# Performance work log

Hardware: AMD Instinct MI355X
Metric: run time of the kernel (lower is better)

Reference implementation:

```python
import jax, jax.numpy as jnp
import numpy as np

LR = 0.1  # inner-loop learning rate from `param - 0.1 * grad`

D = 4096          # memory width d; key/val are (1, d) per docstring
CTX = 512         # loss_context_size: number of keys per update step


def setup_inputs() -> dict:
    key = jax.random.key(0)
    k1, k2, k3 = jax.random.split(key, 3)
    W = jax.random.normal(k1, (D, D), dtype=jnp.float32) / np.sqrt(D)
    keys = jax.random.normal(k2, (CTX, D), dtype=jnp.float32)
    vals = jax.random.normal(k3, (CTX, D), dtype=jnp.float32)
    return {"W": W, "keys": keys, "vals": vals}


def reference(W, keys, vals):
    # OneStep.forward: preds_i = functional_forward(key_i, (W,)) = key_i @ W,
    # loss = MSE(preds, vals); new_W = W - 0.1 * dloss/dW.
    # The per-key loop is batched into a single (CTX, D) x (D, D) matmul.
    def loss_fn(Wp):
        preds = keys @ Wp  # (CTX, D)
        return jnp.mean((preds - vals) ** 2)

    g = jax.grad(loss_fn)(W)
    return W - LR * g
```

## Files before the change

kernel.cpp:

```cpp
#include <hip/hip_runtime.h>
#include <hip/hip_bf16.h>


typedef __bf16 bf16_t;
typedef __bf16 bf16x8 __attribute__((ext_vector_type(8)));
typedef float f32x4 __attribute__((ext_vector_type(4)));

#define D_DIM 4096
#define CTX_N 512
#define UPD_SCALE 9.5367431640625e-8f

__device__ __forceinline__ void gld16(const bf16_t* g, bf16_t* l) {
    __builtin_amdgcn_global_load_lds(
        (const __attribute__((address_space(1))) void*)g,
        (__attribute__((address_space(3))) void*)l, 16, 0, 0);
}

__device__ __forceinline__ void t_body2(
    float* tile, const float* __restrict__ src, bf16_t* __restrict__ dstT,
    bf16_t* __restrict__ dstN, int M, int N, int bx, int by)
{
    const int tid = threadIdx.x;
    const int C0 = bx * 64, R0 = by * 64;
    const int r  = tid >> 2, cs = (tid & 3) * 16;

    const float* s = src + (size_t)(R0 + r) * N + C0 + cs;
    float f[16];
#pragma unroll
    for (int u = 0; u < 4; ++u) {
        const float4 v = ((const float4*)s)[u];
        f[4 * u + 0] = v.x; f[4 * u + 1] = v.y; f[4 * u + 2] = v.z; f[4 * u + 3] = v.w;
    }
#pragma unroll
    for (int u = 0; u < 16; ++u) tile[r * 65 + cs + u] = f[u];

    if (dstN) {
        bf16x8 v0, v1;
#pragma unroll
        for (int u = 0; u < 8; ++u) { v0[u] = (bf16_t)f[u]; v1[u] = (bf16_t)f[8 + u]; }
        bf16_t* d = dstN + (size_t)(R0 + r) * N + C0 + cs;
        *(bf16x8*)d = v0; *(bf16x8*)(d + 8) = v1;
    }
    __syncthreads();

    bf16x8 o0, o1;
#pragma unroll
    for (int u = 0; u < 8; ++u) {
        o0[u] = (bf16_t)tile[(cs + u) * 65 + r];
        o1[u] = (bf16_t)tile[(cs + 8 + u) * 65 + r];
    }
    bf16_t* d = dstT + (size_t)(C0 + r) * M + R0 + cs;
    *(bf16x8*)d = o0; *(bf16x8*)(d + 8) = o1;
}

__global__ __launch_bounds__(256) void t_all(
    const float* __restrict__ W, const float* __restrict__ K,
    const float* __restrict__ V, bf16_t* __restrict__ Wt,
    bf16_t* __restrict__ Kt, bf16_t* __restrict__ Kb, bf16_t* __restrict__ Vt)
{
    __shared__ float tile[64 * 65];
    const int y = blockIdx.y;
    if (y < 64)      t_body2(tile, W, Wt, nullptr, D_DIM, D_DIM, blockIdx.x, y);
    else if (y < 72) t_body2(tile, K, Kt, Kb,      CTX_N, D_DIM, blockIdx.x, y - 64);
    else             t_body2(tile, V, Vt, nullptr, CTX_N, D_DIM, blockIdx.x, y - 72);
}



__global__ __launch_bounds__(512, 2) void k1_residual(
    const bf16_t* __restrict__ Wt, const bf16_t* __restrict__ Kb,
    const bf16_t* __restrict__ Vt, bf16_t* __restrict__ Rt)
{
    __shared__ __align__(16) bf16_t stg[2 * 12288];

    const int tid = threadIdx.x, wave = tid >> 6, lane = tid & 63;
    const int j0 = blockIdx.x * 128, c0 = blockIdx.y * 64;
    const int l15 = lane & 15, quad = lane >> 4;
    const int wm = wave >> 1, wn = wave & 1;

    f32x4 acc[2][2] = {};

    const int smi = wave >> 1, skk = wave & 1;
    const bf16_t* gA1 = Wt + (size_t)(j0 + smi * 16 + l15) * D_DIM + skk * 32 + quad * 8;
    const bf16_t* gA2 = gA1 + (size_t)64 * D_DIM;
    const bf16_t* gB  = Kb + (size_t)(c0 + smi * 16 + l15) * D_DIM + skk * 32 + quad * 8;

    auto stage = [&](int bsel, int t) {
        bf16_t* base = stg + bsel * 12288;
        gld16(gA1 + t * 64, base + (size_t)wave * 512 + lane * 8);
        gld16(gA2 + t * 64, base + (size_t)(8 + wave) * 512 + lane * 8);
        gld16(gB  + t * 64, base + 8192 + (size_t)wave * 512 + lane * 8);
    };

#define K1_COMPUTE(BSEL)                                                     \
    {                                                                        \
        const bf16_t* buf = stg + (BSEL) * 12288;                            \
        bf16x8 a[2][2], b[2][2];                                             \
        _Pragma("unroll")                                                    \
        for (int kk = 0; kk < 2; ++kk)                                       \
            _Pragma("unroll")                                                \
            for (int x = 0; x < 2; ++x) {                                    \
                a[x][kk] = *(const bf16x8*)(                                 \
                    buf + ((wm * 2 + x) * 2 + kk) * 512 + lane * 8);         \
                b[x][kk] = *(const bf16x8*)(                                 \
                    buf + 8192 + ((wn * 2 + x) * 2 + kk) * 512 + lane * 8);  \
            }                                                                \
        _Pragma("unroll")                                                    \
        for (int kk = 0; kk < 2; ++kk)                                       \
            _Pragma("unroll")                                                \
            for (int mi = 0; mi < 2; ++mi)                                   \
                _Pragma("unroll")                                            \
                for (int ni = 0; ni < 2; ++ni)                               \
                    acc[mi][ni] = __builtin_amdgcn_mfma_f32_16x16x32_bf16(   \
                        a[mi][kk], b[ni][kk], acc[mi][ni], 0, 0, 0);         \
    }

    stage(0, 0);
    __syncthreads();
#pragma unroll 1
    for (int t = 0; t < 62; t += 2) {
        stage(1, t + 1);
        __builtin_amdgcn_sched_barrier(0);
        K1_COMPUTE(0);
        __syncthreads();
        stage(0, t + 2);
        __builtin_amdgcn_sched_barrier(0);
        K1_COMPUTE(1);
        __syncthreads();
    }
    stage(1, 63);
    __builtin_amdgcn_sched_barrier(0);
    K1_COMPUTE(0);
    __syncthreads();
    K1_COMPUTE(1);

    {
        const size_t base =
            (size_t)(j0 + wm * 32 + quad * 4) * CTX_N + c0 + wn * 32 + l15;
#pragma unroll
        for (int mi = 0; mi < 2; ++mi)
#pragma unroll
            for (int r = 0; r < 4; ++r) {
                const size_t rowb = base + (size_t)(mi * 16 + r) * CTX_N;
#pragma unroll
                for (int ni = 0; ni < 2; ++ni) {
                    const size_t idx = rowb + ni * 16;
                    Rt[idx] = (bf16_t)(acc[mi][ni][r] - (float)Vt[idx]);
                }
            }
    }
}


#define K2_COMPUTE(BSEL)                                                     \
    {                                                                        \
        const bf16_t* As = (const bf16_t*)(smem + (BSEL) * 16384);           \
        const bf16_t* Bs = (const bf16_t*)(smem + (BSEL) * 16384 + 8192);    \
        bf16x8 af[4], bq[4];                                                 \
        _Pragma("unroll")                                                    \
        for (int mi = 0; mi < 4; ++mi)                                       \
            af[mi] = *(const bf16x8*)(As + (wi + mi * 16 + l15) * 32 + quad * 8); \
        _Pragma("unroll")                                                    \
        for (int ni = 0; ni < 4; ++ni)                                       \
            bq[ni] = *(const bf16x8*)(Bs + (wj + ni * 16 + l15) * 32 + quad * 8); \
        _Pragma("unroll")                                                    \
        for (int mi = 0; mi < 4; ++mi)                                       \
            _Pragma("unroll")                                                \
            for (int ni = 0; ni < 4; ++ni)                                   \
                acc[mi][ni] = __builtin_amdgcn_mfma_f32_16x16x32_bf16(       \
                    af[mi], bq[ni], acc[mi][ni], 0, 0, 0);                   \
    }

__global__ __launch_bounds__(256) void k2_update(
    const bf16_t* __restrict__ Kt, const bf16_t* __restrict__ Rt,
    const float* __restrict__ W, float* __restrict__ out)
{
    __shared__ __align__(16) char smem[32768];

    const int tid = threadIdx.x;

    const int id = blockIdx.x + 32 * blockIdx.y;
    const int xp = (id >> 3) & 31;
    const int yp = (id & 7) + 8 * (id >> 8);
    const int j0 = xp * 128, i0 = yp * 128;

    const int lane = tid & 63, wave = tid >> 6;
    const int wi = (wave >> 1) * 64, wj = (wave & 1) * 64;
    const int l15 = lane & 15, quad = lane >> 4;

    f32x4 acc[4][4] = {};

    const bf16_t* ga = Kt + (size_t)(i0 + (tid >> 2)) * CTX_N + (tid & 3) * 8;
    const bf16_t* gb = Rt + (size_t)(j0 + (tid >> 2)) * CTX_N + (tid & 3) * 8;

    auto stage = [&](int bsel, int cc) {
        bf16_t* la = (bf16_t*)(smem + bsel * 16384) + tid * 8;
        bf16_t* lb = (bf16_t*)(smem + bsel * 16384 + 8192) + tid * 8;
        gld16(ga + cc, la);
        gld16(ga + cc + (size_t)64 * CTX_N, la + 64 * 32);
        gld16(gb + cc, lb);
        gld16(gb + cc + (size_t)64 * CTX_N, lb + 64 * 32);
    };

    stage(0, 0);
    __syncthreads();
#pragma unroll 1
    for (int t = 1; t <= 13; t += 2) {
        stage(1, t * 32);
        __builtin_amdgcn_sched_barrier(0);
        K2_COMPUTE(0);
        __syncthreads();
        stage(0, (t + 1) * 32);
        __builtin_amdgcn_sched_barrier(0);
        K2_COMPUTE(1);
        __syncthreads();
    }
    stage(1, 15 * 32);
    __builtin_amdgcn_sched_barrier(0);
    K2_COMPUTE(0);
    __syncthreads();
    K2_COMPUTE(1);

    const size_t base = (size_t)(i0 + wi + quad * 4) * D_DIM + j0 + wj + l15;
    const float* wp = W + base;
    float*       op = out + base;

    float w0[16], w1[16];
#pragma unroll
    for (int r = 0; r < 4; ++r)
#pragma unroll
        for (int ni = 0; ni < 4; ++ni)
            w0[r * 4 + ni] = wp[(size_t)r * D_DIM + ni * 16];

#pragma unroll
    for (int mi = 0; mi < 4; ++mi) {
        float* wcur = (mi & 1) ? w1 : w0;
        float* wnxt = (mi & 1) ? w0 : w1;
        if (mi < 3) {
#pragma unroll
            for (int r = 0; r < 4; ++r)
#pragma unroll
                for (int ni = 0; ni < 4; ++ni)
                    wnxt[r * 4 + ni] =
                        wp[(size_t)((mi + 1) * 16 + r) * D_DIM + ni * 16];
        }
#pragma unroll
        for (int r = 0; r < 4; ++r)
#pragma unroll
            for (int ni = 0; ni < 4; ++ni)
                op[(size_t)(mi * 16 + r) * D_DIM + ni * 16] =
                    wcur[r * 4 + ni] - UPD_SCALE * acc[mi][ni][r];
    }
}

extern "C" void kernel_launch(void* const* d_in, const int* in_sizes, int n_in,
                              void* d_out, int out_size, void* d_ws, size_t ws_size,
                              hipStream_t stream) {
    const float* W = (const float*)d_in[0];
    const float* K = (const float*)d_in[1];
    const float* V = (const float*)d_in[2];
    float* out = (float*)d_out;

    char* ws = (char*)d_ws;
    bf16_t* Wt = (bf16_t*)(ws);
    bf16_t* Kt = (bf16_t*)(ws + (size_t)32 * 1024 * 1024);
    bf16_t* Kb = (bf16_t*)(ws + (size_t)36 * 1024 * 1024);
    bf16_t* Vt = (bf16_t*)(ws + (size_t)40 * 1024 * 1024);
    bf16_t* Rt = (bf16_t*)(ws + (size_t)44 * 1024 * 1024);

    t_all      <<<dim3(64, 80), 256, 0, stream>>>(W, K, V, Wt, Kt, Kb, Vt);
    k1_residual<<<dim3(32, 8),  512, 0, stream>>>(Wt, Kb, Vt, Rt);
    k2_update  <<<dim3(32, 32), 256, 0, stream>>>(Kt, Rt, W, out);
}
```

Measured before the change: 228.0 us.

## Shrink k1 block tile to 64x64 with XOR-swizzled LDS staging

```diff
diff --git a/kernel.cpp b/kernel.cpp
--- a/kernel.cpp
+++ b/kernel.cpp
@@ -67,44 +67,50 @@
 
 
 
-__global__ __launch_bounds__(512, 2) void k1_residual(
+__global__ __launch_bounds__(256, 2) void k1_residual(
     const bf16_t* __restrict__ Wt, const bf16_t* __restrict__ Kb,
     const bf16_t* __restrict__ Vt, bf16_t* __restrict__ Rt)
 {
-    __shared__ __align__(16) bf16_t stg[2 * 12288];
+    __shared__ __align__(16) bf16_t stg[16384];
 
     const int tid = threadIdx.x, wave = tid >> 6, lane = tid & 63;
-    const int j0 = blockIdx.x * 128, c0 = blockIdx.y * 64;
+    const int j0 = blockIdx.x * 64, c0 = blockIdx.y * 64;
     const int l15 = lane & 15, quad = lane >> 4;
     const int wm = wave >> 1, wn = wave & 1;
 
     f32x4 acc[2][2] = {};
 
-    const int smi = wave >> 1, skk = wave & 1;
-    const bf16_t* gA1 = Wt + (size_t)(j0 + smi * 16 + l15) * D_DIM + skk * 32 + quad * 8;
-    const bf16_t* gA2 = gA1 + (size_t)64 * D_DIM;
-    const bf16_t* gB  = Kb + (size_t)(c0 + smi * 16 + l15) * D_DIM + skk * 32 + quad * 8;
+    const int rl = lane >> 3;
+    const int sl = ((lane & 7) ^ rl) * 8;
+    const bf16_t* gA0 = Wt + (size_t)(j0 + wave * 8      + rl) * D_DIM + sl;
+    const bf16_t* gA1 = Wt + (size_t)(j0 + wave * 8 + 32 + rl) * D_DIM + sl;
+    const bf16_t* gB0 = Kb + (size_t)(c0 + wave * 8      + rl) * D_DIM + sl;
+    const bf16_t* gB1 = Kb + (size_t)(c0 + wave * 8 + 32 + rl) * D_DIM + sl;
 
     auto stage = [&](int bsel, int t) {
-        bf16_t* base = stg + bsel * 12288;
-        gld16(gA1 + t * 64, base + (size_t)wave * 512 + lane * 8);
-        gld16(gA2 + t * 64, base + (size_t)(8 + wave) * 512 + lane * 8);
-        gld16(gB  + t * 64, base + 8192 + (size_t)wave * 512 + lane * 8);
+        bf16_t* buf = stg + bsel * 8192;
+        gld16(gA0 + t * 64, buf + (size_t)wave * 512 + lane * 8);
+        gld16(gA1 + t * 64, buf + (size_t)(wave + 4) * 512 + lane * 8);
+        gld16(gB0 + t * 64, buf + 4096 + (size_t)wave * 512 + lane * 8);
+        gld16(gB1 + t * 64, buf + 4096 + (size_t)(wave + 4) * 512 + lane * 8);
     };
 
 #define K1_COMPUTE(BSEL)                                                     \
     {                                                                        \
-        const bf16_t* buf = stg + (BSEL) * 12288;                            \
+        const bf16_t* buf = stg + (BSEL) * 8192;                             \
+        const int r3 = l15 & 7, uh = l15 >> 3;                               \
         bf16x8 a[2][2], b[2][2];                                             \
         _Pragma("unroll")                                                    \
-        for (int kk = 0; kk < 2; ++kk)                                       \
+        for (int kk = 0; kk < 2; ++kk) {                                     \
+            const int slot = r3 * 8 + ((kk * 4 + quad) ^ r3);                \
             _Pragma("unroll")                                                \
             for (int x = 0; x < 2; ++x) {                                    \
-                a[x][kk] = *(const bf16x8*)(                                 \
-                    buf + ((wm * 2 + x) * 2 + kk) * 512 + lane * 8);         \
-                b[x][kk] = *(const bf16x8*)(                                 \
-                    buf + 8192 + ((wn * 2 + x) * 2 + kk) * 512 + lane * 8);  \
+                const int uA = wm * 4 + x * 2 + uh;                          \
+                const int uB = wn * 4 + x * 2 + uh;                          \
+                a[x][kk] = *(const bf16x8*)(buf + uA * 512 + slot * 8);      \
+                b[x][kk] = *(const bf16x8*)(buf + 4096 + uB * 512 + slot * 8); \
             }                                                                \
+        }                                                                    \
         _Pragma("unroll")                                                    \
         for (int kk = 0; kk < 2; ++kk)                                       \
             _Pragma("unroll")                                                \
@@ -269,6 +275,6 @@
     bf16_t* Rt = (bf16_t*)(ws + (size_t)44 * 1024 * 1024);
 
     t_all      <<<dim3(64, 80), 256, 0, stream>>>(W, K, V, Wt, Kt, Kb, Vt);
-    k1_residual<<<dim3(32, 8),  512, 0, stream>>>(Wt, Kb, Vt, Rt);
+    k1_residual<<<dim3(64, 8),  256, 0, stream>>>(Wt, Kb, Vt, Rt);
     k2_update  <<<dim3(32, 32), 256, 0, stream>>>(Kt, Rt, W, out);
 }
```

Measured after the change: 193.8 us. 15.0% less time.
